# Kernel tuning notes

Hardware: AMD Instinct MI355X
Metric: run time of the kernel (lower is better)

## Reference

```python
import jax, jax.numpy as jnp
import numpy as np

H = 128  # hidden size, hardcoded by the module's reshapes


def setup_inputs() -> dict:
    key = jax.random.key(0)
    ks = jax.random.split(key, 6)
    return {
        "x_t": jax.random.normal(ks[0], (1, 512), dtype=jnp.float32),
        "h0": jax.random.normal(ks[1], (2, 1, H), dtype=jnp.float32),
        "w_ih_f": jax.random.normal(ks[2], (3 * H, 512), dtype=jnp.float32) * 0.05,
        "w_hh_f": jax.random.normal(ks[3], (3 * H, H), dtype=jnp.float32) * 0.05,
        "b_ih_f": jax.random.normal(ks[4], (3 * H,), dtype=jnp.float32) * 0.05,
        "b_hh_f": jax.random.normal(ks[5], (3 * H,), dtype=jnp.float32) * 0.05,
    }


def reference(x_t, h0, w_ih_f, w_hh_f, b_ih_f, b_hh_f):
    # forward-direction hidden state: h0[0] -> (1, H)
    h_f = h0[0].reshape(1, H)
    x = x_t.reshape(1, 512)
    # two GEMVs producing all three gates at once: (1, 3H)
    gates_x = x @ w_ih_f.T + b_ih_f
    gates_h = h_f @ w_hh_f.T + b_hh_f
    r_x, z_x, n_x = jnp.split(gates_x, 3, axis=1)
    r_h, z_h, n_h = jnp.split(gates_h, 3, axis=1)
    r_t = jax.nn.sigmoid(r_x + r_h)
    z_t = jax.nn.sigmoid(z_x + z_h)
    n_t = jnp.tanh(n_x + r_t * n_h)
    h_new = (1.0 - z_t) * n_t + z_t * h_f
    return h_new.reshape(1, H)
```

## Files before the change

### kernel.cpp

```cpp
#include <hip/hip_runtime.h>
#include <math.h>

#define H 128

__device__ __forceinline__ float wave_reduce_sum(float v) {
    #pragma unroll
    for (int m = 32; m >= 1; m >>= 1) v += __shfl_xor(v, m, 64);
    return v;
}

__device__ __forceinline__ float sigmoidf(float x) {
    return 1.0f / (1.0f + __expf(-x));
}

__global__ __launch_bounds__(192) void gru_fwd_cell_kernel(
    const float* __restrict__ x,
    const float* __restrict__ h0,
    const float* __restrict__ w_ih,
    const float* __restrict__ w_hh,
    const float* __restrict__ b_ih,
    const float* __restrict__ b_hh,
    float* __restrict__ out)
{
    const int j    = blockIdx.x;
    const int tid  = threadIdx.x;
    const int wave = tid >> 6;
    const int lane = tid & 63;

    const int row = j + (wave << 7);

    const float4* wih4 = reinterpret_cast<const float4*>(w_ih + (size_t)row * 512);
    const float4* x4   = reinterpret_cast<const float4*>(x);
    float accX = 0.0f;
    #pragma unroll
    for (int s = 0; s < 2; ++s) {
        const int idx = lane + (s << 6);
        float4 wv = wih4[idx];
        float4 xv = x4[idx];
        accX += wv.x * xv.x + wv.y * xv.y + wv.z * xv.z + wv.w * xv.w;
    }

    const float2* whh2 = reinterpret_cast<const float2*>(w_hh + (size_t)row * H);
    const float2* h2   = reinterpret_cast<const float2*>(h0);
    float accH;
    {
        float2 wv = whh2[lane];
        float2 hv = h2[lane];
        accH = wv.x * hv.x + wv.y * hv.y;
    }

    accX = wave_reduce_sum(accX);
    accH = wave_reduce_sum(accH);

    __shared__ float sX[3];
    __shared__ float sH[3];
    if (lane == 0) {
        sX[wave] = accX;
        sH[wave] = accH;
    }
    __syncthreads();

    if (tid == 0) {
        const float hj = h0[j];
        const float r = sigmoidf(sX[0] + b_ih[j]       + sH[0] + b_hh[j]);
        const float z = sigmoidf(sX[1] + b_ih[j + 128] + sH[1] + b_hh[j + 128]);
        const float n = tanhf(sX[2] + b_ih[j + 256] + r * (sH[2] + b_hh[j + 256]));
        out[j] = (1.0f - z) * n + z * hj;
    }
}

extern "C" void kernel_launch(void* const* d_in, const int* in_sizes, int n_in,
                              void* d_out, int out_size, void* d_ws, size_t ws_size,
                              hipStream_t stream) {
    const float* x    = (const float*)d_in[0];
    const float* h0   = (const float*)d_in[1];
    const float* w_ih = (const float*)d_in[2];
    const float* w_hh = (const float*)d_in[3];
    const float* b_ih = (const float*)d_in[4];
    const float* b_hh = (const float*)d_in[5];
    float* out = (float*)d_out;

    gru_fwd_cell_kernel<<<H, 192, 0, stream>>>(x, h0, w_ih, w_hh, b_ih, b_hh, out);
}
```

Before: 9.967 us.

## Use one wave per output handling all three gates, dropping shared-memory sync

Each block now runs a single 64-lane wave that computes the r, z and n gate dot products for its output element, instead of three waves with one gate each. The six reductions are interleaved in one shuffle loop, which removes the shared-memory exchange and the __syncthreads, and the bias and h loads are hoisted to the start so they issue early. In exchange each wave carries three times the memory traffic and per-lane work, and the launch has fewer total waves to hide memory latency.

```diff
diff --git a/kernel.cpp b/kernel.cpp
--- a/kernel.cpp
+++ b/kernel.cpp
@@ -3,17 +3,11 @@
 
 #define H 128
 
-__device__ __forceinline__ float wave_reduce_sum(float v) {
-    #pragma unroll
-    for (int m = 32; m >= 1; m >>= 1) v += __shfl_xor(v, m, 64);
-    return v;
-}
-
-__device__ __forceinline__ float sigmoidf(float x) {
+__device__ __forceinline__ float sigmoidf_(float x) {
     return 1.0f / (1.0f + __expf(-x));
 }
 
-__global__ __launch_bounds__(192) void gru_fwd_cell_kernel(
+__global__ __launch_bounds__(64) void gru_fwd_cell_kernel(
     const float* __restrict__ x,
     const float* __restrict__ h0,
     const float* __restrict__ w_ih,
@@ -23,48 +17,51 @@
     float* __restrict__ out)
 {
     const int j    = blockIdx.x;
-    const int tid  = threadIdx.x;
-    const int wave = tid >> 6;
-    const int lane = tid & 63;
+    const int lane = threadIdx.x;
 
-    const int row = j + (wave << 7);
+    const float bih_r = b_ih[j];
+    const float bih_z = b_ih[j + 128];
+    const float bih_n = b_ih[j + 256];
+    const float bhh_r = b_hh[j];
+    const float bhh_z = b_hh[j + 128];
+    const float bhh_n = b_hh[j + 256];
+    const float hj    = h0[j];
 
-    const float4* wih4 = reinterpret_cast<const float4*>(w_ih + (size_t)row * 512);
-    const float4* x4   = reinterpret_cast<const float4*>(x);
-    float accX = 0.0f;
+    const float4* x4 = reinterpret_cast<const float4*>(x);
+    const float4 xv0 = x4[lane];
+    const float4 xv1 = x4[lane + 64];
+
+    const float2* h2 = reinterpret_cast<const float2*>(h0);
+    const float2 hv  = h2[lane];
+
+    float aX[3], aH[3];
     #pragma unroll
-    for (int s = 0; s < 2; ++s) {
-        const int idx = lane + (s << 6);
-        float4 wv = wih4[idx];
-        float4 xv = x4[idx];
-        accX += wv.x * xv.x + wv.y * xv.y + wv.z * xv.z + wv.w * xv.w;
+    for (int g = 0; g < 3; ++g) {
+        const int row = j + (g << 7);
+        const float4* w4 = reinterpret_cast<const float4*>(w_ih + (size_t)row * 512);
+        const float4 wa = w4[lane];
+        const float4 wb = w4[lane + 64];
+        aX[g] = wa.x * xv0.x + wa.y * xv0.y + wa.z * xv0.z + wa.w * xv0.w
+              + wb.x * xv1.x + wb.y * xv1.y + wb.z * xv1.z + wb.w * xv1.w;
+
+        const float2* wh2 = reinterpret_cast<const float2*>(w_hh + (size_t)row * H);
+        const float2 wh = wh2[lane];
+        aH[g] = wh.x * hv.x + wh.y * hv.y;
     }
 
-    const float2* whh2 = reinterpret_cast<const float2*>(w_hh + (size_t)row * H);
-    const float2* h2   = reinterpret_cast<const float2*>(h0);
-    float accH;
-    {
-        float2 wv = whh2[lane];
-        float2 hv = h2[lane];
-        accH = wv.x * hv.x + wv.y * hv.y;
+    #pragma unroll
+    for (int m = 32; m >= 1; m >>= 1) {
+        #pragma unroll
+        for (int g = 0; g < 3; ++g) {
+            aX[g] += __shfl_xor(aX[g], m, 64);
+            aH[g] += __shfl_xor(aH[g], m, 64);
+        }
     }
 
-    accX = wave_reduce_sum(accX);
-    accH = wave_reduce_sum(accH);
-
-    __shared__ float sX[3];
-    __shared__ float sH[3];
     if (lane == 0) {
-        sX[wave] = accX;
-        sH[wave] = accH;
-    }
-    __syncthreads();
-
-    if (tid == 0) {
-        const float hj = h0[j];
-        const float r = sigmoidf(sX[0] + b_ih[j]       + sH[0] + b_hh[j]);
-        const float z = sigmoidf(sX[1] + b_ih[j + 128] + sH[1] + b_hh[j + 128]);
-        const float n = tanhf(sX[2] + b_ih[j + 256] + r * (sH[2] + b_hh[j + 256]));
+        const float r = sigmoidf_(aX[0] + bih_r + aH[0] + bhh_r);
+        const float z = sigmoidf_(aX[1] + bih_z + aH[1] + bhh_z);
+        const float n = tanhf(aX[2] + bih_n + r * (aH[2] + bhh_n));
         out[j] = (1.0f - z) * n + z * hj;
     }
 }
@@ -80,5 +77,5 @@
     const float* b_hh = (const float*)d_in[5];
     float* out = (float*)d_out;
 
-    gru_fwd_cell_kernel<<<H, 192, 0, stream>>>(x, h0, w_ih, w_hh, b_ih, b_hh, out);
+    gru_fwd_cell_kernel<<<H, 64, 0, stream>>>(x, h0, w_ih, w_hh, b_ih, b_hh, out);
 }
```

Result: slower. 12.74 us (+27.8%).
